# Optimization experiments

Hardware: AMD Instinct MI355X
Metric: run time of the kernel (lower is better)

Reference implementation:

```python
import jax, jax.numpy as jnp
import numpy as np

N = 100000          # nodes (src == target here)
E = 1600000         # edges, avg degree 16
C_IN = 128
C_OUT = 128
R = 7               # num_edge_types
T = 4               # num_node_types


def setup_inputs() -> dict:
    key = jax.random.key(0)
    ks = jax.random.split(key, 7)
    x = jax.random.normal(ks[0], (N, C_IN), dtype=jnp.float32)
    edge_index = jax.random.randint(ks[1], (2, E), 0, N, dtype=jnp.int32)
    edge_type = jax.random.randint(ks[2], (E,), 0, R, dtype=jnp.int32)
    target_node_type = jax.random.randint(ks[3], (N,), 0, T, dtype=jnp.int32)
    # Linear weights: rel_lins (no bias), root_lins (with bias); torch Linear: y = x @ W.T + b
    rel_w = jax.random.normal(ks[4], (R, C_OUT, C_IN), dtype=jnp.float32) * (1.0 / np.sqrt(C_IN))
    root_w = jax.random.normal(ks[5], (T, C_OUT, C_IN), dtype=jnp.float32) * (1.0 / np.sqrt(C_IN))
    root_b = jax.random.normal(ks[6], (T, C_OUT), dtype=jnp.float32) * 0.01
    return {"x": x, "edge_index": edge_index, "edge_type": edge_type,
            "target_node_type": target_node_type,
            "rel_w": rel_w, "root_w": root_w, "root_b": root_b}


def reference(x, edge_index, edge_type, target_node_type, rel_w, root_w, root_b):
    # Per-edge-type gather -> (bias-free) linear -> scatter-mean.
    # linear commutes with mean (no bias), so aggregate first, then apply W_r.
    n = x.shape[0]
    src, dst = edge_index[0], edge_index[1]
    x_j = x[src]                                   # [E, C_in] gather
    seg = dst.astype(jnp.int32) * R + edge_type    # fused (node, edge_type) segment id
    sums = jax.ops.segment_sum(x_j, seg, num_segments=n * R).reshape(n, R, C_IN)
    cnt = jax.ops.segment_sum(jnp.ones((x_j.shape[0],), x.dtype), seg,
                              num_segments=n * R).reshape(n, R)
    means = sums / jnp.maximum(cnt, 1.0)[:, :, None]   # zero rows stay zero (PyG mean of empty = 0)
    out = jnp.einsum('nrc,roc->no', means, rel_w)       # sum_r rel_lins[r](mean_r)
    # Per-node-type root linear with bias (small loop over T=4 types).
    for t in range(T):
        m = (target_node_type == t).astype(x.dtype)[:, None]
        out = out + m * (x @ root_w[t].T + root_b[t])
    return out
```

## Files before the change

kernel.cpp:

```cpp
#include <hip/hip_runtime.h>

#define N_NODES 100000
#define N_EDGES 1600000
#define C_DIM   128
#define R_TYPES 7
#define T_TYPES 4
#define SEGS    (N_NODES * R_TYPES)
#define NB_E    (N_EDGES / 256)
#define NB_N    ((N_NODES + 255) / 256)
#define XP_ROWS 100096
#define DST_PART 12500

#define OFF_CNTI   0ull
#define OFF_INV    2800000ull
#define OFF_DOFF   5600000ull
#define OFF_CURS   6000004ull
#define OFF_MISC   6400004ull
#define OFF_PERM   6400132ull
#define PERM_CAP   100288
#define N_PERM_BLOCKS 1567
#define OFF_BLKN   6801284ull
#define OFF_BSUM   6813796ull
#define OFF_ESRC   6815360ull
#define OFF_XP     13215360ull
#define OFF_WF     38839936ull
#define OFF_XWB    39069312ull
#define XWB_PLANE  ((size_t)XP_ROWS * 128)
#define FULL_NEED  218441344ull
#define FB_NEED    64693888ull

typedef __attribute__((ext_vector_type(8))) short short8;
typedef __attribute__((ext_vector_type(4))) float f32x4;

__device__ inline unsigned short f2bf(float f) {
    unsigned int u = __float_as_uint(f);
    u += 0x7fffu + ((u >> 16) & 1u);
    return (unsigned short)(u >> 16);
}
__device__ inline float bf2f(unsigned int h) { return __uint_as_float(h << 16); }

__global__ void edge_hist(const int* __restrict__ ei, const int* __restrict__ et,
                          int* __restrict__ cnti) {
    int e = blockIdx.x * 256 + threadIdx.x;
    atomicAdd(&cnti[ei[N_EDGES + e] * R_TYPES + et[e]], 1);
}

__global__ void inv_kernel(const int* __restrict__ cnti, float* __restrict__ inv) {
    int i = blockIdx.x * blockDim.x + threadIdx.x;
    if (i < SEGS) inv[i] = 1.0f / (float)max(cnti[i], 1);
}

__global__ void dst_scan1(const int* __restrict__ cnti, int* __restrict__ dst_off,
                          int* __restrict__ bsum) {
    __shared__ int sbuf[256];
    int tid = threadIdx.x;
    int i = blockIdx.x * 256 + tid;
    int v = 0;
    if (i < N_NODES) {
        #pragma unroll
        for (int r = 0; r < R_TYPES; ++r) v += cnti[i * R_TYPES + r];
    }
    sbuf[tid] = v;
    __syncthreads();
    #pragma unroll
    for (int off = 1; off < 256; off <<= 1) {
        int t = (tid >= off) ? sbuf[tid - off] : 0;
        __syncthreads();
        sbuf[tid] += t;
        __syncthreads();
    }
    int incl = sbuf[tid];
    if (i < N_NODES) dst_off[i] = incl - v;
    if (tid == 255) bsum[blockIdx.x] = incl;
}

__global__ void seg_scan2(int* __restrict__ bsum, int nb) {
    __shared__ int sbuf[256];
    int tid = threadIdx.x;
    int running = 0;
    for (int c0 = 0; c0 < nb; c0 += 256) {
        int b = c0 + tid;
        int v = (b < nb) ? bsum[b] : 0;
        sbuf[tid] = v;
        __syncthreads();
        #pragma unroll
        for (int off = 1; off < 256; off <<= 1) {
            int t = (tid >= off) ? sbuf[tid - off] : 0;
            __syncthreads();
            sbuf[tid] += t;
            __syncthreads();
        }
        int incl = sbuf[tid];
        int tot = sbuf[255];
        __syncthreads();
        if (b < nb) bsum[b] = running + incl - v;
        running += tot;
    }
}

__global__ void dst_scan3(int* __restrict__ dst_off, int* __restrict__ cursor,
                          const int* __restrict__ bsum) {
    int i = blockIdx.x * 256 + threadIdx.x;
    if (i < N_NODES) {
        int val = dst_off[i] + bsum[blockIdx.x];
        dst_off[i] = val;
        cursor[i] = val;
    }
    if (i == 0) dst_off[N_NODES] = N_EDGES;
}

__global__ void place_edges(const int* __restrict__ ei, const int* __restrict__ et,
                            int* __restrict__ cursor, int* __restrict__ esrc) {
    int p = blockIdx.x & 7;
    int e = (blockIdx.x >> 3) * 256 + threadIdx.x;
    int d = ei[N_EDGES + e];
    if (d / DST_PART != p) return;
    int pos = atomicAdd(&cursor[d], 1);
    int r = et[e];
    esrc[pos] = (r << 20) | (r * XP_ROWS + ei[e]);
}

__global__ void node_hist(const int* __restrict__ tnt, int* __restrict__ blk_n) {
    __shared__ int h[8];
    int tid = threadIdx.x;
    if (tid < 8) h[tid] = 0;
    __syncthreads();
    int n = blockIdx.x * 256 + tid;
    if (n < N_NODES) atomicAdd(&h[tnt[n]], 1);
    __syncthreads();
    if (tid < T_TYPES) blk_n[blockIdx.x * 8 + tid] = h[tid];
}

__global__ void scan_blocks(int* __restrict__ blk, int nb, int* __restrict__ total) {
    __shared__ int sbuf[256];
    int r = blockIdx.x;
    int tid = threadIdx.x;
    int running = 0;
    for (int c0 = 0; c0 < nb; c0 += 256) {
        int b = c0 + tid;
        int v = (b < nb) ? blk[b * 8 + r] : 0;
        sbuf[tid] = v;
        __syncthreads();
        #pragma unroll
        for (int off = 1; off < 256; off <<= 1) {
            int t = (tid >= off) ? sbuf[tid - off] : 0;
            __syncthreads();
            sbuf[tid] += t;
            __syncthreads();
        }
        int incl = sbuf[tid];
        int chunk_total = sbuf[255];
        __syncthreads();
        if (b < nb) blk[b * 8 + r] = running + incl - v;
        running += chunk_total;
    }
    if (tid == 0) total[r] = running;
}

__global__ void offsets_kernel(int* misc) {
    if (threadIdx.x == 0 && blockIdx.x == 0) {
        int s = 0;
        for (int t = 0; t < T_TYPES; ++t) {
            misc[4 + t] = s;
            s += ((misc[t] + 63) / 64) * 64;
        }
    }
}

__global__ void node_scatter(const int* __restrict__ tnt, const int* __restrict__ misc,
                             const int* __restrict__ blk_n, int* __restrict__ perm) {
    __shared__ int h[8];
    int tid = threadIdx.x;
    if (tid < 8) h[tid] = 0;
    __syncthreads();
    int n = blockIdx.x * 256 + tid;
    if (n < N_NODES) {
        int t = tnt[n];
        int rank = atomicAdd(&h[t], 1);
        perm[misc[4 + t] + blk_n[blockIdx.x * 8 + t] + rank] = n;
    }
}

__global__ void cvt_x_frag(const float* __restrict__ x, unsigned short* __restrict__ xp) {
    int id = blockIdx.x * 256 + threadIdx.x;
    int n = id >> 4, ko = id & 15;
    short8 o;
    if (n < N_NODES) {
        const float4* px = (const float4*)(x + (size_t)n * C_DIM + ko * 8);
        float4 a = px[0], b = px[1];
        o[0] = (short)f2bf(a.x); o[1] = (short)f2bf(a.y);
        o[2] = (short)f2bf(a.z); o[3] = (short)f2bf(a.w);
        o[4] = (short)f2bf(b.x); o[5] = (short)f2bf(b.y);
        o[6] = (short)f2bf(b.z); o[7] = (short)f2bf(b.w);
    } else {
        o = (short8)0;
    }
    size_t off = (size_t)(n >> 4) * 2048 + (ko >> 2) * 512 + (ko & 3) * 128 + (n & 15) * 8;
    *(short8*)(xp + off) = o;
}

__global__ void cvt_w_frag(const float* __restrict__ rel_w, unsigned short* __restrict__ wf) {
    int id = blockIdx.x * 256 + threadIdx.x;
    if (id >= R_TYPES * 128 * 16) return;
    int r = id >> 11, rest = id & 2047;
    int o = rest >> 4, ko = rest & 15;
    const float4* pw = (const float4*)(rel_w + (size_t)r * 16384 + o * 128 + ko * 8);
    float4 a = pw[0], b = pw[1];
    short8 v;
    v[0] = (short)f2bf(a.x); v[1] = (short)f2bf(a.y);
    v[2] = (short)f2bf(a.z); v[3] = (short)f2bf(a.w);
    v[4] = (short)f2bf(b.x); v[5] = (short)f2bf(b.y);
    v[6] = (short)f2bf(b.z); v[7] = (short)f2bf(b.w);
    size_t off = (size_t)r * 16384 + (o >> 4) * 2048 + (ko >> 2) * 512 + (ko & 3) * 128 + (o & 15) * 8;
    *(short8*)(wf + off) = v;
}

__launch_bounds__(256)
__global__ void xw_gemm_all(const unsigned short* __restrict__ xp,
                            const unsigned short* __restrict__ wf,
                            unsigned short* __restrict__ xwb7) {
    int wave = threadIdx.x >> 6, lane = threadIdx.x & 63;
    int m0 = blockIdx.x * 128;

    short8 a[4][2];
    #pragma unroll
    for (int kb = 0; kb < 4; ++kb)
        #pragma unroll
        for (int rt = 0; rt < 2; ++rt) {
            size_t rtile = (size_t)blockIdx.x * 8 + wave * 2 + rt;
            a[kb][rt] = *(const short8*)(xp + rtile * 2048 + kb * 512 + lane * 8);
        }

    int col = lane & 15, rq = (lane >> 4) * 4;
    for (int r = 0; r < R_TYPES; ++r) {
        const unsigned short* wr = wf + (size_t)r * 16384;
        unsigned short* xwb = xwb7 + (size_t)r * XWB_PLANE;
        #pragma unroll
        for (int ct = 0; ct < 8; ++ct) {
            f32x4 acc0 = (f32x4)0.0f, acc1 = (f32x4)0.0f;
            #pragma unroll
            for (int kb = 0; kb < 4; ++kb) {
                short8 b = *(const short8*)(wr + (size_t)ct * 2048 + kb * 512 + lane * 8);
                acc0 = __builtin_amdgcn_mfma_f32_16x16x32_bf16(a[kb][0], b, acc0, 0, 0, 0);
                acc1 = __builtin_amdgcn_mfma_f32_16x16x32_bf16(a[kb][1], b, acc1, 0, 0, 0);
            }
            #pragma unroll
            for (int i = 0; i < 4; ++i) {
                int n0 = m0 + wave * 32 + rq + i;
                if (n0 < N_NODES)
                    xwb[(size_t)n0 * C_DIM + ct * 16 + col] = f2bf(acc0[i]);
                int n1 = n0 + 16;
                if (n1 < N_NODES)
                    xwb[(size_t)n1 * C_DIM + ct * 16 + col] = f2bf(acc1[i]);
            }
        }
    }
}

__launch_bounds__(256)
__global__ void xw_gemm_mfma(const unsigned short* __restrict__ xp,
                             const unsigned short* __restrict__ wf,
                             unsigned short* __restrict__ xwb, int r) {
    int wave = threadIdx.x >> 6, lane = threadIdx.x & 63;
    int m0 = blockIdx.x * 128;
    const unsigned short* wr = wf + (size_t)r * 16384;

    short8 a[4][2];
    #pragma unroll
    for (int kb = 0; kb < 4; ++kb)
        #pragma unroll
        for (int rt = 0; rt < 2; ++rt) {
            size_t rtile = (size_t)blockIdx.x * 8 + wave * 2 + rt;
            a[kb][rt] = *(const short8*)(xp + rtile * 2048 + kb * 512 + lane * 8);
        }

    int col = lane & 15, rq = (lane >> 4) * 4;
    #pragma unroll
    for (int ct = 0; ct < 8; ++ct) {
        f32x4 acc0 = (f32x4)0.0f, acc1 = (f32x4)0.0f;
        #pragma unroll
        for (int kb = 0; kb < 4; ++kb) {
            short8 b = *(const short8*)(wr + (size_t)ct * 2048 + kb * 512 + lane * 8);
            acc0 = __builtin_amdgcn_mfma_f32_16x16x32_bf16(a[kb][0], b, acc0, 0, 0, 0);
            acc1 = __builtin_amdgcn_mfma_f32_16x16x32_bf16(a[kb][1], b, acc1, 0, 0, 0);
        }
        #pragma unroll
        for (int i = 0; i < 4; ++i) {
            int n0 = m0 + wave * 32 + rq + i;
            if (n0 < N_NODES)
                xwb[(size_t)n0 * C_DIM + ct * 16 + col] = f2bf(acc0[i]);
            int n1 = n0 + 16;
            if (n1 < N_NODES)
                xwb[(size_t)n1 * C_DIM + ct * 16 + col] = f2bf(acc1[i]);
        }
    }
}

__global__ void gather_fused(const int* __restrict__ dst_off, const int* __restrict__ esrc,
                             const float* __restrict__ inv,
                             const unsigned short* __restrict__ xwb7,
                             float* __restrict__ out) {
    int wave = threadIdx.x >> 6, lane = threadIdx.x & 63;
    int d = blockIdx.x * 4 + wave;
    if (d >= N_NODES) return;
    int o0 = dst_off[d], o1 = dst_off[d + 1];
    int q = lane >> 4;
    int l16 = lane & 15;
    const float* invd = inv + d * R_TYPES;
    float acc[8];
    #pragma unroll
    for (int j = 0; j < 8; ++j) acc[j] = 0.f;

    int e = o0;
    int pkA = 0, pkB = 0;
    bool run = (e + 8 <= o1);
    if (run) { pkA = esrc[e + q]; pkB = esrc[e + 4 + q]; }
    while (run) {
        uint4 rA = *(const uint4*)(xwb7 + (size_t)(pkA & 0xFFFFF) * C_DIM + l16 * 8);
        uint4 rB = *(const uint4*)(xwb7 + (size_t)(pkB & 0xFFFFF) * C_DIM + l16 * 8);
        float sA = invd[pkA >> 20];
        float sB = invd[pkB >> 20];
        e += 8;
        run = (e + 8 <= o1);
        if (run) { pkA = esrc[e + q]; pkB = esrc[e + 4 + q]; }
        acc[0] += bf2f(rA.x & 0xffffu) * sA;  acc[1] += bf2f(rA.x >> 16) * sA;
        acc[2] += bf2f(rA.y & 0xffffu) * sA;  acc[3] += bf2f(rA.y >> 16) * sA;
        acc[4] += bf2f(rA.z & 0xffffu) * sA;  acc[5] += bf2f(rA.z >> 16) * sA;
        acc[6] += bf2f(rA.w & 0xffffu) * sA;  acc[7] += bf2f(rA.w >> 16) * sA;
        acc[0] += bf2f(rB.x & 0xffffu) * sB;  acc[1] += bf2f(rB.x >> 16) * sB;
        acc[2] += bf2f(rB.y & 0xffffu) * sB;  acc[3] += bf2f(rB.y >> 16) * sB;
        acc[4] += bf2f(rB.z & 0xffffu) * sB;  acc[5] += bf2f(rB.z >> 16) * sB;
        acc[6] += bf2f(rB.w & 0xffffu) * sB;  acc[7] += bf2f(rB.w >> 16) * sB;
    }
    for (; e < o1; e += 4) {
        int idx = e + q;
        bool valid = idx < o1;
        int pk = esrc[valid ? idx : e];
        uint4 rw = *(const uint4*)(xwb7 + (size_t)(pk & 0xFFFFF) * C_DIM + l16 * 8);
        float s = valid ? invd[pk >> 20] : 0.0f;
        acc[0] += bf2f(rw.x & 0xffffu) * s;  acc[1] += bf2f(rw.x >> 16) * s;
        acc[2] += bf2f(rw.y & 0xffffu) * s;  acc[3] += bf2f(rw.y >> 16) * s;
        acc[4] += bf2f(rw.z & 0xffffu) * s;  acc[5] += bf2f(rw.z >> 16) * s;
        acc[6] += bf2f(rw.w & 0xffffu) * s;  acc[7] += bf2f(rw.w >> 16) * s;
    }

    #pragma unroll
    for (int j = 0; j < 8; ++j) {
        acc[j] += __shfl_xor(acc[j], 16);
        acc[j] += __shfl_xor(acc[j], 32);
    }
    if (lane < 16) {
        float4* po = (float4*)(out + (size_t)d * C_DIM + l16 * 8);
        po[0] = make_float4(acc[0], acc[1], acc[2], acc[3]);
        po[1] = make_float4(acc[4], acc[5], acc[6], acc[7]);
    }
}

__global__ void gather_rel_f(const int* __restrict__ dst_off, const int* __restrict__ esrc,
                             const float* __restrict__ inv,
                             const unsigned short* __restrict__ xwb,
                             float* __restrict__ out, int rf) {
    int wave = threadIdx.x >> 6, lane = threadIdx.x & 63;
    int d = blockIdx.x * 4 + wave;
    if (d >= N_NODES) return;
    int o0 = dst_off[d], o1 = dst_off[d + 1];
    float ax = 0.0f, ay = 0.0f;
    bool any = false;
    for (int e = o0; e < o1; ++e) {
        int pk = esrc[e];
        if ((pk >> 20) != rf) continue;
        any = true;
        int src = (pk & 0xFFFFF) - rf * XP_ROWS;
        unsigned int row = *(const unsigned int*)(xwb + (size_t)src * C_DIM + lane * 2);
        ax += bf2f(row & 0xffffu);
        ay += bf2f(row >> 16);
    }
    if (!any) return;
    float sc = inv[d * R_TYPES + rf];
    float2* po = (float2*)(out + (size_t)d * C_DIM) + lane;
    float2 v = *po;
    v.x += ax * sc;
    v.y += ay * sc;
    *po = v;
}

#define ASTR 33
#define BSTR 132
__launch_bounds__(256, 2)
__global__ void root_gemm(const float* __restrict__ x, const float* __restrict__ root_w,
                          const float* __restrict__ root_b, const int* __restrict__ tnt,
                          const int* __restrict__ perm, float* __restrict__ out) {
    __shared__ int   pidx[64];
    __shared__ float As[64 * ASTR];
    __shared__ float Bs[32 * BSTR];
    int tid = threadIdx.x;
    if (tid < 64) pidx[tid] = perm[blockIdx.x * 64 + tid];
    __syncthreads();
    if (pidx[0] < 0) return;
    int t = tnt[pidx[0]];
    int tx = tid & 15;
    int ty = tid >> 4;
    float acc[4][8];
    #pragma unroll
    for (int i = 0; i < 4; ++i)
        #pragma unroll
        for (int j = 0; j < 8; ++j) acc[i][j] = 0.0f;

    for (int kb = 0; kb < 4; ++kb) {
        #pragma unroll
        for (int p = 0; p < 2; ++p) {
            int idx = p * 256 + tid;
            int row = idx >> 3;
            int cc  = (idx & 7) * 4;
            int node = pidx[row];
            float4 v = make_float4(0.f, 0.f, 0.f, 0.f);
            if (node >= 0)
                v = *(const float4*)(x + (size_t)node * C_DIM + kb * 32 + cc);
            As[row * ASTR + cc + 0] = v.x;
            As[row * ASTR + cc + 1] = v.y;
            As[row * ASTR + cc + 2] = v.z;
            As[row * ASTR + cc + 3] = v.w;
        }
        #pragma unroll
        for (int p = 0; p < 4; ++p) {
            int idx = p * 256 + tid;
            int o  = idx >> 3;
            int cc = (idx & 7) * 4;
            float4 v = *(const float4*)(root_w + ((size_t)t * 128 + o) * 128 + kb * 32 + cc);
            Bs[(cc + 0) * BSTR + o] = v.x;
            Bs[(cc + 1) * BSTR + o] = v.y;
            Bs[(cc + 2) * BSTR + o] = v.z;
            Bs[(cc + 3) * BSTR + o] = v.w;
        }
        __syncthreads();
        #pragma unroll
        for (int k = 0; k < 32; ++k) {
            float a[4];
            #pragma unroll
            for (int i = 0; i < 4; ++i) a[i] = As[(ty * 4 + i) * ASTR + k];
            float4 b0 = *(const float4*)&Bs[k * BSTR + tx * 4];
            float4 b1 = *(const float4*)&Bs[k * BSTR + 64 + tx * 4];
            float b[8] = {b0.x, b0.y, b0.z, b0.w, b1.x, b1.y, b1.z, b1.w};
            #pragma unroll
            for (int i = 0; i < 4; ++i)
                #pragma unroll
                for (int j = 0; j < 8; ++j) acc[i][j] += a[i] * b[j];
        }
        __syncthreads();
    }
    float4 bias0 = *(const float4*)(root_b + (size_t)t * 128 + tx * 4);
    float4 bias1 = *(const float4*)(root_b + (size_t)t * 128 + 64 + tx * 4);
    #pragma unroll
    for (int i = 0; i < 4; ++i) {
        int node = pidx[ty * 4 + i];
        if (node < 0) continue;
        float* po = out + (size_t)node * C_DIM;
        float4 v0 = *(float4*)(po + tx * 4);
        float4 v1 = *(float4*)(po + 64 + tx * 4);
        v0.x += acc[i][0] + bias0.x;  v0.y += acc[i][1] + bias0.y;
        v0.z += acc[i][2] + bias0.z;  v0.w += acc[i][3] + bias0.w;
        v1.x += acc[i][4] + bias1.x;  v1.y += acc[i][5] + bias1.y;
        v1.z += acc[i][6] + bias1.z;  v1.w += acc[i][7] + bias1.w;
        *(float4*)(po + tx * 4) = v0;
        *(float4*)(po + 64 + tx * 4) = v1;
    }
}

extern "C" void kernel_launch(void* const* d_in, const int* in_sizes, int n_in,
                              void* d_out, int out_size, void* d_ws, size_t ws_size,
                              hipStream_t stream) {
    const float* x      = (const float*)d_in[0];
    const int*   ei     = (const int*)d_in[1];
    const int*   et     = (const int*)d_in[2];
    const int*   tnt    = (const int*)d_in[3];
    const float* rel_w  = (const float*)d_in[4];
    const float* root_w = (const float*)d_in[5];
    const float* root_b = (const float*)d_in[6];
    float* out = (float*)d_out;

    char* ws = (char*)d_ws;
    int*   cnti    = (int*)(ws + OFF_CNTI);
    float* inv     = (float*)(ws + OFF_INV);
    int*   dst_off = (int*)(ws + OFF_DOFF);
    int*   cursor  = (int*)(ws + OFF_CURS);
    int*   misc    = (int*)(ws + OFF_MISC);
    int*   perm    = (int*)(ws + OFF_PERM);
    int*   blk_n   = (int*)(ws + OFF_BLKN);
    int*   bsum    = (int*)(ws + OFF_BSUM);
    int*   esrc    = (int*)(ws + OFF_ESRC);
    unsigned short* xp  = (unsigned short*)(ws + OFF_XP);
    unsigned short* wf  = (unsigned short*)(ws + OFF_WF);
    unsigned short* xwb = (unsigned short*)(ws + OFF_XWB);

    const bool full = (ws_size >= FULL_NEED);

    hipMemsetAsync(ws + OFF_CNTI, 0, SEGS * sizeof(int), stream);
    hipMemsetAsync(ws + OFF_MISC, 0, 32 * sizeof(int), stream);
    hipMemsetAsync(ws + OFF_PERM, 0xFF, (size_t)PERM_CAP * sizeof(int), stream);
    if (!full)
        hipMemsetAsync(d_out, 0, (size_t)out_size * sizeof(float), stream);

    edge_hist  <<<NB_E, 256, 0, stream>>>(ei, et, cnti);
    inv_kernel <<<(SEGS + 255) / 256, 256, 0, stream>>>(cnti, inv);
    dst_scan1  <<<NB_N, 256, 0, stream>>>(cnti, dst_off, bsum);
    seg_scan2  <<<1, 256, 0, stream>>>(bsum, NB_N);
    dst_scan3  <<<NB_N, 256, 0, stream>>>(dst_off, cursor, bsum);
    place_edges<<<NB_E * 8, 256, 0, stream>>>(ei, et, cursor, esrc);

    node_hist  <<<NB_N, 256, 0, stream>>>(tnt, blk_n);
    scan_blocks<<<T_TYPES, 256, 0, stream>>>(blk_n, NB_N, misc + 0);
    offsets_kernel<<<1, 64, 0, stream>>>(misc);
    node_scatter<<<NB_N, 256, 0, stream>>>(tnt, misc, blk_n, perm);

    cvt_x_frag<<<(XP_ROWS * 16) / 256, 256, 0, stream>>>(x, xp);
    cvt_w_frag<<<56, 256, 0, stream>>>(rel_w, wf);

    if (full) {
        xw_gemm_all <<<XP_ROWS / 128, 256, 0, stream>>>(xp, wf, xwb);
        gather_fused<<<(N_NODES + 3) / 4, 256, 0, stream>>>(dst_off, esrc, inv, xwb, out);
    } else {
        for (int r = 0; r < R_TYPES; ++r) {
            xw_gemm_mfma<<<XP_ROWS / 128, 256, 0, stream>>>(xp, wf, xwb, r);
            gather_rel_f<<<(N_NODES + 3) / 4, 256, 0, stream>>>(dst_off, esrc, inv, xwb, out, r);
        }
    }
    root_gemm<<<N_PERM_BLOCKS, 256, 0, stream>>>(x, root_w, root_b, tnt, perm, out);
}
```

Measured before the change: 490.0 us.

## Replace FP32 root GEMM with split-bf16 MFMA kernel using prepacked weights

Replaces the scalar FP32 shared-memory root-linear GEMM with an MFMA kernel that splits both x and root_w into bf16 hi/lo parts and runs three bf16 MFMAs per k-block to keep roughly FP32 accuracy. Root weights are pre-converted into MFMA fragment layout, stored in workspace that reuses the count buffer, which is already consumed by that point. This removes LDS staging and the scalar FMA loop. In exchange it adds a small conversion kernel, scattered 4-byte read-modify-write output stores, and a small loss of precision.

```diff
diff --git a/kernel.cpp b/kernel.cpp
--- a/kernel.cpp
+++ b/kernel.cpp
@@ -28,6 +28,7 @@
 #define XWB_PLANE  ((size_t)XP_ROWS * 128)
 #define FULL_NEED  218441344ull
 #define FB_NEED    64693888ull
+#define OFF_WRF    OFF_CNTI
 
 typedef __attribute__((ext_vector_type(8))) short short8;
 typedef __attribute__((ext_vector_type(4))) float f32x4;
@@ -213,6 +214,26 @@
     v[6] = (short)f2bf(b.z); v[7] = (short)f2bf(b.w);
     size_t off = (size_t)r * 16384 + (o >> 4) * 2048 + (ko >> 2) * 512 + (ko & 3) * 128 + (o & 15) * 8;
     *(short8*)(wf + off) = v;
+}
+
+__global__ void cvt_rootw_frag(const float* __restrict__ root_w, unsigned short* __restrict__ wrf) {
+    int id = blockIdx.x * 256 + threadIdx.x;
+    if (id >= T_TYPES * 128 * 16) return;
+    int t = id >> 11, rest = id & 2047;
+    int o = rest >> 4, ko = rest & 15;
+    const float4* pw = (const float4*)(root_w + (size_t)t * 16384 + o * 128 + ko * 8);
+    float4 a = pw[0], b = pw[1];
+    float v[8] = {a.x, a.y, a.z, a.w, b.x, b.y, b.z, b.w};
+    short8 hi, lo;
+    #pragma unroll
+    for (int j = 0; j < 8; ++j) {
+        unsigned short h = f2bf(v[j]);
+        hi[j] = (short)h;
+        lo[j] = (short)f2bf(v[j] - bf2f(h));
+    }
+    size_t off = (size_t)t * 16384 + (o >> 4) * 2048 + (ko >> 2) * 512 + (ko & 3) * 128 + (o & 15) * 8;
+    *(short8*)(wrf + off) = hi;
+    *(short8*)(wrf + (size_t)T_TYPES * 16384 + off) = lo;
 }
 
 __launch_bounds__(256)
@@ -384,85 +405,64 @@
     *po = v;
 }
 
-#define ASTR 33
-#define BSTR 132
-__launch_bounds__(256, 2)
-__global__ void root_gemm(const float* __restrict__ x, const float* __restrict__ root_w,
+__launch_bounds__(256)
+__global__ void root_mfma(const float* __restrict__ x, const unsigned short* __restrict__ wrf,
                           const float* __restrict__ root_b, const int* __restrict__ tnt,
                           const int* __restrict__ perm, float* __restrict__ out) {
-    __shared__ int   pidx[64];
-    __shared__ float As[64 * ASTR];
-    __shared__ float Bs[32 * BSTR];
+    __shared__ int pidx[64];
     int tid = threadIdx.x;
+    int wave = tid >> 6, lane = tid & 63;
     if (tid < 64) pidx[tid] = perm[blockIdx.x * 64 + tid];
     __syncthreads();
     if (pidx[0] < 0) return;
     int t = tnt[pidx[0]];
-    int tx = tid & 15;
-    int ty = tid >> 4;
-    float acc[4][8];
-    #pragma unroll
-    for (int i = 0; i < 4; ++i)
-        #pragma unroll
-        for (int j = 0; j < 8; ++j) acc[i][j] = 0.0f;
-
+
+    int node = pidx[wave * 16 + (lane & 15)];
+    int k0 = (lane >> 4) * 8;
+    short8 ah[4], al[4];
+    #pragma unroll
     for (int kb = 0; kb < 4; ++kb) {
-        #pragma unroll
-        for (int p = 0; p < 2; ++p) {
-            int idx = p * 256 + tid;
-            int row = idx >> 3;
-            int cc  = (idx & 7) * 4;
-            int node = pidx[row];
-            float4 v = make_float4(0.f, 0.f, 0.f, 0.f);
-            if (node >= 0)
-                v = *(const float4*)(x + (size_t)node * C_DIM + kb * 32 + cc);
-            As[row * ASTR + cc + 0] = v.x;
-            As[row * ASTR + cc + 1] = v.y;
-            As[row * ASTR + cc + 2] = v.z;
-            As[row * ASTR + cc + 3] = v.w;
-        }
-        #pragma unroll
-        for (int p = 0; p < 4; ++p) {
-            int idx = p * 256 + tid;
-            int o  = idx >> 3;
-            int cc = (idx & 7) * 4;
-            float4 v = *(const float4*)(root_w + ((size_t)t * 128 + o) * 128 + kb * 32 + cc);
-            Bs[(cc + 0) * BSTR + o] = v.x;
-            Bs[(cc + 1) * BSTR + o] = v.y;
-            Bs[(cc + 2) * BSTR + o] = v.z;
-            Bs[(cc + 3) * BSTR + o] = v.w;
-        }
-        __syncthreads();
-        #pragma unroll
-        for (int k = 0; k < 32; ++k) {
-            float a[4];
+        float v[8];
+        if (node >= 0) {
+            const float4* px = (const float4*)(x + (size_t)node * C_DIM + kb * 32 + k0);
+            float4 p0 = px[0], p1 = px[1];
+            v[0] = p0.x; v[1] = p0.y; v[2] = p0.z; v[3] = p0.w;
+            v[4] = p1.x; v[5] = p1.y; v[6] = p1.z; v[7] = p1.w;
+        } else {
             #pragma unroll
-            for (int i = 0; i < 4; ++i) a[i] = As[(ty * 4 + i) * ASTR + k];
-            float4 b0 = *(const float4*)&Bs[k * BSTR + tx * 4];
-            float4 b1 = *(const float4*)&Bs[k * BSTR + 64 + tx * 4];
-            float b[8] = {b0.x, b0.y, b0.z, b0.w, b1.x, b1.y, b1.z, b1.w};
-            #pragma unroll
-            for (int i = 0; i < 4; ++i)
-                #pragma unroll
-                for (int j = 0; j < 8; ++j) acc[i][j] += a[i] * b[j];
-        }
-        __syncthreads();
-    }
-    float4 bias0 = *(const float4*)(root_b + (size_t)t * 128 + tx * 4);
-    float4 bias1 = *(const float4*)(root_b + (size_t)t * 128 + 64 + tx * 4);
-    #pragma unroll
-    for (int i = 0; i < 4; ++i) {
-        int node = pidx[ty * 4 + i];
-        if (node < 0) continue;
-        float* po = out + (size_t)node * C_DIM;
-        float4 v0 = *(float4*)(po + tx * 4);
-        float4 v1 = *(float4*)(po + 64 + tx * 4);
-        v0.x += acc[i][0] + bias0.x;  v0.y += acc[i][1] + bias0.y;
-        v0.z += acc[i][2] + bias0.z;  v0.w += acc[i][3] + bias0.w;
-        v1.x += acc[i][4] + bias1.x;  v1.y += acc[i][5] + bias1.y;
-        v1.z += acc[i][6] + bias1.z;  v1.w += acc[i][7] + bias1.w;
-        *(float4*)(po + tx * 4) = v0;
-        *(float4*)(po + 64 + tx * 4) = v1;
+            for (int j = 0; j < 8; ++j) v[j] = 0.0f;
+        }
+        #pragma unroll
+        for (int j = 0; j < 8; ++j) {
+            unsigned short h = f2bf(v[j]);
+            ah[kb][j] = (short)h;
+            al[kb][j] = (short)f2bf(v[j] - bf2f(h));
+        }
+    }
+
+    const unsigned short* wh = wrf + (size_t)t * 16384;
+    const unsigned short* wl = wrf + (size_t)(T_TYPES + t) * 16384;
+    int col = lane & 15, rq = (lane >> 4) * 4;
+    #pragma unroll
+    for (int ct = 0; ct < 8; ++ct) {
+        f32x4 acc = (f32x4)0.0f;
+        #pragma unroll
+        for (int kb = 0; kb < 4; ++kb) {
+            short8 bh = *(const short8*)(wh + ct * 2048 + kb * 512 + lane * 8);
+            short8 bl = *(const short8*)(wl + ct * 2048 + kb * 512 + lane * 8);
+            acc = __builtin_amdgcn_mfma_f32_16x16x32_bf16(ah[kb], bh, acc, 0, 0, 0);
+            acc = __builtin_amdgcn_mfma_f32_16x16x32_bf16(al[kb], bh, acc, 0, 0, 0);
+            acc = __builtin_amdgcn_mfma_f32_16x16x32_bf16(ah[kb], bl, acc, 0, 0, 0);
+        }
+        float bias = root_b[t * 128 + ct * 16 + col];
+        #pragma unroll
+        for (int i = 0; i < 4; ++i) {
+            int nr = pidx[wave * 16 + rq + i];
+            if (nr >= 0) {
+                float* po = out + (size_t)nr * C_DIM + ct * 16 + col;
+                *po += acc[i] + bias;
+            }
+        }
     }
 }
 
@@ -491,6 +491,7 @@
     unsigned short* xp  = (unsigned short*)(ws + OFF_XP);
     unsigned short* wf  = (unsigned short*)(ws + OFF_WF);
     unsigned short* xwb = (unsigned short*)(ws + OFF_XWB);
+    unsigned short* wrf = (unsigned short*)(ws + OFF_WRF);
 
     const bool full = (ws_size >= FULL_NEED);
 
@@ -506,6 +507,8 @@
     seg_scan2  <<<1, 256, 0, stream>>>(bsum, NB_N);
     dst_scan3  <<<NB_N, 256, 0, stream>>>(dst_off, cursor, bsum);
     place_edges<<<NB_E * 8, 256, 0, stream>>>(ei, et, cursor, esrc);
+
+    cvt_rootw_frag<<<32, 256, 0, stream>>>(root_w, wrf);
 
     node_hist  <<<NB_N, 256, 0, stream>>>(tnt, blk_n);
     scan_blocks<<<T_TYPES, 256, 0, stream>>>(blk_n, NB_N, misc + 0);
@@ -524,5 +527,5 @@
             gather_rel_f<<<(N_NODES + 3) / 4, 256, 0, stream>>>(dst_off, esrc, inv, xwb, out, r);
         }
     }
-    root_gemm<<<N_PERM_BLOCKS, 256, 0, stream>>>(x, root_w, root_b, tnt, perm, out);
-}
+    root_mfma<<<N_PERM_BLOCKS, 256, 0, stream>>>(x, wrf, root_b, tnt, perm, out);
+}
```

Result: no change. 494.1 us (+0.8%).
